# Performance work log

Measured on AMD Instinct MI355X. Metric: run time of the kernel, lower is better.

## Reference

```python
import jax, jax.numpy as jnp
import numpy as np


def setup_inputs() -> dict:
    key = jax.random.key(0)
    N, nH, D, L, P = 2, 8, 32, 4, 4
    shapes = np.array([[92, 92], [46, 46], [23, 23], [12, 12]], dtype=np.int64)
    areas = shapes[:, 0] * shapes[:, 1]
    Lin = int(areas.sum())  # 11253
    Lq = Lin  # encoder self-attention
    k1, k2, k3 = jax.random.split(key, 3)
    value = jax.random.normal(k1, (N, Lin, nH, D), dtype=jnp.float32)
    sampling_locations = jax.random.uniform(k2, (N, Lq, nH, L, P, 2), dtype=jnp.float32)
    aw = jax.random.uniform(k3, (N, Lq, nH, L, P), dtype=jnp.float32)
    attention_weights = aw / aw.sum(axis=(-2, -1), keepdims=True)  # softmax-normalized over L*P
    spatial_shapes = jnp.asarray(shapes)
    starts = np.concatenate([[0], np.cumsum(areas)[:-1]])
    level_start_index = jnp.asarray(starts, dtype=jnp.int64)
    return dict(value=value, spatial_shapes=spatial_shapes,
                level_start_index=level_start_index,
                sampling_locations=sampling_locations,
                attention_weights=attention_weights)


def _gather2d(v_nh, xi, yi, Hl, Wl):
    # v_nh: [N, nH, Hl*Wl, D]; xi, yi: [N, Lq, nH, P] int32 pixel coords
    N, Lq, nH, P = xi.shape
    valid = (xi >= 0) & (xi < Wl) & (yi >= 0) & (yi < Hl)
    xc = jnp.clip(xi, 0, Wl - 1)
    yc = jnp.clip(yi, 0, Hl - 1)
    idx = (yc * Wl + xc).transpose(0, 2, 1, 3).reshape(N, nH, Lq * P)
    vals = jax.vmap(jax.vmap(lambda v, i: v[i]))(v_nh, idx)  # [N, nH, Lq*P, D]
    vals = vals.reshape(N, nH, Lq, P, -1).transpose(0, 2, 1, 3, 4)  # [N, Lq, nH, P, D]
    return vals * valid[..., None].astype(vals.dtype)


def reference(value, spatial_shapes, level_start_index, sampling_locations, attention_weights):
    # ms_deform_attn core: per-level bilinear sampling (align_corners=False,
    # zero padding) at learned locations, weighted sum over levels and points.
    shapes_np = np.asarray(spatial_shapes)
    starts_np = np.asarray(level_start_index)
    N, Lin, nH, D = value.shape
    _, Lq, _, L, P, _ = sampling_locations.shape
    out = jnp.zeros((N, Lq, nH, D), dtype=value.dtype)
    for lvl in range(L):
        Hl, Wl = int(shapes_np[lvl, 0]), int(shapes_np[lvl, 1])
        s = int(starts_np[lvl])
        v_nh = value[:, s:s + Hl * Wl].transpose(0, 2, 1, 3)  # [N, nH, Hl*Wl, D]
        loc = sampling_locations[:, :, :, lvl]  # [N, Lq, nH, P, 2]
        # grid_sample convention: normalized [0,1] -> pixel coord, align_corners=False
        x = loc[..., 0] * Wl - 0.5
        y = loc[..., 1] * Hl - 0.5
        x0f = jnp.floor(x); y0f = jnp.floor(y)
        dx = x - x0f; dy = y - y0f
        x0 = x0f.astype(jnp.int32); y0 = y0f.astype(jnp.int32)
        x1 = x0 + 1; y1 = y0 + 1
        w00 = ((1.0 - dx) * (1.0 - dy))[..., None]
        w01 = (dx * (1.0 - dy))[..., None]
        w10 = ((1.0 - dx) * dy)[..., None]
        w11 = (dx * dy)[..., None]
        samp = (w00 * _gather2d(v_nh, x0, y0, Hl, Wl)
                + w01 * _gather2d(v_nh, x1, y0, Hl, Wl)
                + w10 * _gather2d(v_nh, x0, y1, Hl, Wl)
                + w11 * _gather2d(v_nh, x1, y1, Hl, Wl))  # [N, Lq, nH, P, D]
        aw_l = attention_weights[:, :, :, lvl]  # [N, Lq, nH, P]
        out = out + (samp * aw_l[..., None]).sum(axis=3)
    return out.reshape(N, Lq, nH * D)
```

## Files before the change

### kernel.cpp

```cpp
#include <hip/hip_runtime.h>

#define NH 8
#define DD 32
#define LL 4
#define PP 4

typedef float  f32x4  __attribute__((ext_vector_type(4)));
typedef float  f32x2  __attribute__((ext_vector_type(2)));
typedef int    i32x4  __attribute__((ext_vector_type(4)));
typedef _Float16 half4v __attribute__((ext_vector_type(4)));

__global__ __launch_bounds__(256) void conv_kernel(
    const float* __restrict__ value, _Float16* __restrict__ vh,
    int Lin, int spx, int nSlabs)
{
    const int xcd  = blockIdx.x & 7;
    const int blk  = blockIdx.x >> 3;
    const int sw   = blk % spx;
    const int seg  = blk / spx;
    const int slab = xcd * spx + sw;
    if (slab >= nSlabs) return;
    const int i = seg * 256 + threadIdx.x;
    if (i >= Lin * 8) return;
    const int d4  = i & 7;
    const int pos = i >> 3;
    const int n   = slab >> 3;
    const int h   = slab & 7;

    const f32x4 v = __builtin_nontemporal_load(
        (const f32x4*)(value + (((size_t)n * Lin + pos) * NH + h) * DD + d4 * 4));
    half4v o;
    o.x = (_Float16)v.x; o.y = (_Float16)v.y; o.z = (_Float16)v.z; o.w = (_Float16)v.w;
    *(half4v*)(vh + ((size_t)slab * Lin + pos) * DD + d4 * 4) = o;
}

#define FMAMIX_LO(ACC, DW, W) \
    asm("v_fma_mix_f32 %0, %1, %2, %0 op_sel:[0,0,0] op_sel_hi:[1,0,0]" \
        : "+v"(ACC) : "v"(DW), "v"(W))
#define FMAMIX_HI(ACC, DW, W) \
    asm("v_fma_mix_f32 %0, %1, %2, %0 op_sel:[1,0,0] op_sel_hi:[1,0,0]" \
        : "+v"(ACC) : "v"(DW), "v"(W))

#define SB() __builtin_amdgcn_sched_barrier(0)

__global__ __attribute__((amdgpu_flat_work_group_size(256, 256)))
__attribute__((amdgpu_waves_per_eu(4)))
void msda_fwd_h(
    const _Float16* __restrict__ vh,
    const int*   __restrict__ ssh,
    const int*   __restrict__ lsi,
    const float* __restrict__ sloc,
    const float* __restrict__ aw,
    float*       __restrict__ out,
    int N, int Lq, int Lin, int spx, int nSlabs)
{
    __shared__ i32x4 ent[32 * 39];

    const int xcd   = blockIdx.x & 7;
    const int blk   = blockIdx.x >> 3;
    const int sw    = blk % spx;
    const int chunk = blk / spx;
    const int slab  = xcd * spx + sw;
    if (slab >= nSlabs) return;

    const int t  = threadIdx.x;
    const int u  = t >> 3;
    const int j  = t & 7;
    const int q  = chunk * 32 + u;
    const int qc = min(q, Lq - 1);
    const int n  = slab >> 3;
    const int h  = slab & 7;

    {
        const size_t nqh = ((size_t)n * Lq + qc) * NH + h;
        const int l = j >> 1;
        const bool is64 = (ssh[1] == 0);
        const int W = is64 ? ssh[4 * l + 2] : ssh[2 * l + 1];
        const int H = is64 ? ssh[4 * l]     : ssh[2 * l];
        const int S = is64 ? lsi[2 * l]     : lsi[l];
        const f32x4 lc = __builtin_nontemporal_load((const f32x4*)sloc + nqh * 8 + j);
        const f32x2 av = __builtin_nontemporal_load((const f32x2*)aw + nqh * 8 + j);
        const float fW = (float)W, fH = (float)H;
        const int rowb  = W * (DD * 2);
        const int sbase = S * (DD * 2);
#pragma unroll
        for (int pt = 0; pt < 2; ++pt) {
            const float x  = lc[2 * pt]     * fW - 0.5f;
            const float y  = lc[2 * pt + 1] * fH - 0.5f;
            const float wq = av[pt];
            const float x0f = floorf(x), y0f = floorf(y);
            const int x0 = (int)x0f, y0 = (int)y0f;
            const float dx = x - x0f, dy = y - y0f;
            const int x1 = x0 + 1, y1 = y0 + 1;
            const bool vx0 = (x0 >= 0) & (x0 < W), vx1 = (x1 >= 0) & (x1 < W);
            const bool vy0 = (y0 >= 0) & (y0 < H), vy1 = (y1 >= 0) & (y1 < H);
            const int cx0 = min(max(x0, 0), W - 1), cx1 = min(max(x1, 0), W - 1);
            const int cy0 = min(max(y0, 0), H - 1), cy1 = min(max(y1, 0), H - 1);
            const float wx0 = (1.f - dx) * wq * (vx0 ? 1.f : 0.f);
            const float wx1 = dx         * wq * (vx1 ? 1.f : 0.f);
            const float ty  = (1.f - dy) * (vy0 ? 1.f : 0.f);
            const float by  = dy         * (vy1 ? 1.f : 0.f);
            const int rt = cy0 * rowb + sbase;
            const int rb = cy1 * rowb + sbase;
            i32x4 e0, e1;
            e0.x = rt + cx0 * (DD * 2);  e0.y = rb + cx0 * (DD * 2);
            e0.z = __float_as_int(wx0 * ty);  e0.w = __float_as_int(wx0 * by);
            e1.x = rt + cx1 * (DD * 2);  e1.y = rb + cx1 * (DD * 2);
            e1.z = __float_as_int(wx1 * ty);  e1.w = __float_as_int(wx1 * by);
            const int base = u * 39 + 5 * j + 2 * pt;
            ent[base]     = e0;
            ent[base + 1] = e1;
        }
    }
    __syncthreads();
    if (q >= Lq) return;

    const int side = j >> 2;
    const int cg   = j & 3;
    const char* __restrict__ sb =
        (const char*)vh + (size_t)slab * Lin * (DD * 2) + cg * 16;
    const int ub = u * 39 + side;

    float acc[8];
#pragma unroll
    for (int k = 0; k < 8; ++k) acc[k] = 0.f;

#define RD(b, E) { \
    E[0] = ent[ub + 10 * (b) + 0]; \
    E[1] = ent[ub + 10 * (b) + 2]; \
    E[2] = ent[ub + 10 * (b) + 5]; \
    E[3] = ent[ub + 10 * (b) + 7]; }
#define LD(E, V) _Pragma("unroll") \
    for (int i = 0; i < 4; ++i) { \
        V[2*i]   = *(const i32x4*)(sb + (unsigned)E[i].x); \
        V[2*i+1] = *(const i32x4*)(sb + (unsigned)E[i].y); }
#define AC(E, V) _Pragma("unroll") \
    for (int i = 0; i < 4; ++i) { \
        const float wt = __int_as_float(E[i].z); \
        const float wb = __int_as_float(E[i].w); \
        _Pragma("unroll") for (int d = 0; d < 4; ++d) { \
            FMAMIX_LO(acc[2*d],   V[2*i][d],   wt); \
            FMAMIX_HI(acc[2*d+1], V[2*i][d],   wt); \
            FMAMIX_LO(acc[2*d],   V[2*i+1][d], wb); \
            FMAMIX_HI(acc[2*d+1], V[2*i+1][d], wb); } }

    i32x4 E0[4], E1[4], E2[4], E3[4];
    i32x4 V0[8], V1[8];
    RD(0, E0) RD(1, E1)
    SB();
    LD(E0, V0) LD(E1, V1)
    SB();
    AC(E0, V0)
    RD(2, E2)
    SB();
    LD(E2, V0)
    SB();
    AC(E1, V1)
    RD(3, E3)
    SB();
    LD(E3, V1)
    SB();
    AC(E2, V0)
    AC(E3, V1)

#pragma unroll
    for (int k = 0; k < 8; ++k)
        acc[k] += __shfl_xor(acc[k], 4);

    f32x4 st;
    st.x = acc[side * 4 + 0];
    st.y = acc[side * 4 + 1];
    st.z = acc[side * 4 + 2];
    st.w = acc[side * 4 + 3];
    const size_t onqh = ((size_t)n * Lq + q) * NH + h;
    __builtin_nontemporal_store(st, (f32x4*)(out + onqh * DD + cg * 8 + side * 4));
}

__global__ __launch_bounds__(256) void msda_fwd_f32(
    const float* __restrict__ value,
    const int*   __restrict__ spatial_shapes,
    const int*   __restrict__ level_start,
    const float* __restrict__ sloc,
    const float* __restrict__ aw,
    float*       __restrict__ out,
    int N, int Lq, int Lin, int total)
{
    int tid = blockIdx.x * blockDim.x + threadIdx.x;
    if (tid >= total) return;
    const int c  = tid & 7;
    const int h  = (tid >> 3) & 7;
    const int nq = tid >> 6;
    const int n  = nq / Lq;
    const bool is64 = (spatial_shapes[1] == 0);
    int Hs[LL], Ws[LL], Ss[LL];
#pragma unroll
    for (int l = 0; l < LL; ++l) {
        if (is64) { Hs[l] = spatial_shapes[4*l]; Ws[l] = spatial_shapes[4*l+2]; Ss[l] = level_start[2*l]; }
        else      { Hs[l] = spatial_shapes[2*l]; Ws[l] = spatial_shapes[2*l+1]; Ss[l] = level_start[l]; }
    }
    const size_t nqh = (size_t)nq * NH + h;
    const float* loc_p = sloc + nqh * (LL * PP * 2);
    const float* aw_p  = aw   + nqh * (LL * PP);
    float4 acc = make_float4(0.f, 0.f, 0.f, 0.f);
#pragma unroll
    for (int l = 0; l < LL; ++l) {
        const int H = Hs[l], W = Ws[l];
        const float* vb = value + (((size_t)n * Lin + Ss[l]) * NH + h) * DD + c * 4;
#pragma unroll
        for (int p = 0; p < PP; ++p) {
            const int jj = l * PP + p;
            const float x = loc_p[2*jj] * (float)W - 0.5f;
            const float y = loc_p[2*jj+1] * (float)H - 0.5f;
            const float w = aw_p[jj];
            const float x0f = floorf(x), y0f = floorf(y);
            const int x0 = (int)x0f, y0 = (int)y0f, x1 = x0+1, y1 = y0+1;
            const float dx = x - x0f, dy = y - y0f;
            const bool vx0 = x0>=0 && x0<W, vx1 = x1>=0 && x1<W;
            const bool vy0 = y0>=0 && y0<H, vy1 = y1>=0 && y1<H;
            const int cx0 = min(max(x0,0),W-1), cx1 = min(max(x1,0),W-1);
            const int cy0 = min(max(y0,0),H-1), cy1 = min(max(y1,0),H-1);
            const float w00 = (1.f-dx)*(1.f-dy)*w*((vx0&&vy0)?1.f:0.f);
            const float w01 = dx*(1.f-dy)*w*((vx1&&vy0)?1.f:0.f);
            const float w10 = (1.f-dx)*dy*w*((vx0&&vy1)?1.f:0.f);
            const float w11 = dx*dy*w*((vx1&&vy1)?1.f:0.f);
            const float4 v00 = *(const float4*)(vb + (size_t)(cy0*W+cx0)*(NH*DD));
            const float4 v01 = *(const float4*)(vb + (size_t)(cy0*W+cx1)*(NH*DD));
            const float4 v10 = *(const float4*)(vb + (size_t)(cy1*W+cx0)*(NH*DD));
            const float4 v11 = *(const float4*)(vb + (size_t)(cy1*W+cx1)*(NH*DD));
            acc.x += w00*v00.x + w01*v01.x + w10*v10.x + w11*v11.x;
            acc.y += w00*v00.y + w01*v01.y + w10*v10.y + w11*v11.y;
            acc.z += w00*v00.z + w01*v01.z + w10*v10.z + w11*v11.z;
            acc.w += w00*v00.w + w01*v01.w + w10*v10.w + w11*v11.w;
        }
    }
    *(float4*)(out + nqh * DD + c * 4) = acc;
}

extern "C" void kernel_launch(void* const* d_in, const int* in_sizes, int n_in,
                              void* d_out, int out_size, void* d_ws, size_t ws_size,
                              hipStream_t stream)
{
    const float* value = (const float*)d_in[0];
    const int*   ss    = (const int*)  d_in[1];
    const int*   lsi   = (const int*)  d_in[2];
    const float* sloc  = (const float*)d_in[3];
    const float* aw    = (const float*)d_in[4];
    float* out = (float*)d_out;

    const int N = 2;
    const int Lq  = in_sizes[4] / (N * NH * LL * PP);
    const int Lin = in_sizes[0] / (N * NH * DD);

    const size_t need = (size_t)N * NH * Lin * DD * sizeof(_Float16);
    if (ws_size >= need) {
        _Float16* vh = (_Float16*)d_ws;
        const int nSlabs = N * NH;
        const int spx    = (nSlabs + 7) / 8;
        const int segs   = (Lin * 8 + 255) / 256;
        conv_kernel<<<8 * spx * segs, 256, 0, stream>>>(value, vh, Lin, spx, nSlabs);

        const int chunks = (Lq + 31) / 32;
        const int grid   = 8 * spx * chunks;
        msda_fwd_h<<<grid, 256, 0, stream>>>(vh, ss, lsi, sloc, aw, out,
                                             N, Lq, Lin, spx, nSlabs);
    } else {
        const int total = N * Lq * NH * 8;
        msda_fwd_f32<<<(total + 255) / 256, 256, 0, stream>>>(value, ss, lsi, sloc, aw, out,
                                                              N, Lq, Lin, total);
    }
}
```

Before: 131.7 us.

## Stage small pyramid levels of value slab into LDS for gathers

Copies the fp16 value data for levels 2 and 3 (the small 23x23 and 12x12 maps, about 42 KB per head slab) into shared memory at block start. Gathers for those levels then read LDS instead of global memory, while levels 0 and 1 still gather from global memory. The gather schedule is restructured so the global loads for levels 0/1 are in flight while the LDS-based accumulation runs. Waves-per-EU drops to 2 to fit the large LDS footprint. The cost is an extra bulk copy per block of 32 queries and lower occupancy.

Result: slower. 148.2 us (+12.6%).

```diff
diff --git a/kernel.cpp b/kernel.cpp
--- a/kernel.cpp
+++ b/kernel.cpp
@@ -4,6 +4,7 @@
 #define DD 32
 #define LL 4
 #define PP 4
+#define STAGE_BYTES 43072
 
 typedef float  f32x4  __attribute__((ext_vector_type(4)));
 typedef float  f32x2  __attribute__((ext_vector_type(2)));
@@ -44,7 +45,7 @@
 #define SB() __builtin_amdgcn_sched_barrier(0)
 
 __global__ __attribute__((amdgpu_flat_work_group_size(256, 256)))
-__attribute__((amdgpu_waves_per_eu(4)))
+__attribute__((amdgpu_waves_per_eu(2)))
 void msda_fwd_h(
     const _Float16* __restrict__ vh,
     const int*   __restrict__ ssh,
@@ -55,6 +56,7 @@
     int N, int Lq, int Lin, int spx, int nSlabs)
 {
     __shared__ i32x4 ent[32 * 39];
+    __shared__ i32x4 stage4[STAGE_BYTES / 16];
 
     const int xcd   = blockIdx.x & 7;
     const int blk   = blockIdx.x >> 3;
@@ -71,10 +73,29 @@
     const int n  = slab >> 3;
     const int h  = slab & 7;
 
+    const bool is64 = (ssh[1] == 0);
+    const int  S2v  = is64 ? lsi[4] : lsi[2];
+    const int  stB  = (Lin - S2v) * (DD * 2);
+    const bool staged = (stB > 0) && (stB <= STAGE_BYTES);
+
+    if (staged) {
+        const char* src = (const char*)vh + ((size_t)slab * Lin + S2v) * (DD * 2);
+        i32x4 tmp[11];
+#pragma unroll
+        for (int k = 0; k < 11; ++k) {
+            const int off = t * 16 + k * 4096;
+            if (off < stB) tmp[k] = *(const i32x4*)(src + off);
+        }
+#pragma unroll
+        for (int k = 0; k < 11; ++k) {
+            const int off = t * 16 + k * 4096;
+            if (off < stB) *(i32x4*)((char*)stage4 + off) = tmp[k];
+        }
+    }
+
     {
         const size_t nqh = ((size_t)n * Lq + qc) * NH + h;
         const int l = j >> 1;
-        const bool is64 = (ssh[1] == 0);
         const int W = is64 ? ssh[4 * l + 2] : ssh[2 * l + 1];
         const int H = is64 ? ssh[4 * l]     : ssh[2 * l];
         const int S = is64 ? lsi[2 * l]     : lsi[l];
@@ -82,7 +103,7 @@
         const f32x2 av = __builtin_nontemporal_load((const f32x2*)aw + nqh * 8 + j);
         const float fW = (float)W, fH = (float)H;
         const int rowb  = W * (DD * 2);
-        const int sbase = S * (DD * 2);
+        const int sbase = (staged && j >= 4) ? (S - S2v) * (DD * 2) : S * (DD * 2);
 #pragma unroll
         for (int pt = 0; pt < 2; ++pt) {
             const float x  = lc[2 * pt]     * fW - 0.5f;
@@ -119,6 +140,7 @@
     const int cg   = j & 3;
     const char* __restrict__ sb =
         (const char*)vh + (size_t)slab * Lin * (DD * 2) + cg * 16;
+    const char* __restrict__ stg = (const char*)stage4 + cg * 16;
     const int ub = u * 39 + side;
 
     float acc[8];
@@ -134,6 +156,10 @@
     for (int i = 0; i < 4; ++i) { \
         V[2*i]   = *(const i32x4*)(sb + (unsigned)E[i].x); \
         V[2*i+1] = *(const i32x4*)(sb + (unsigned)E[i].y); }
+#define LLD(E, V) _Pragma("unroll") \
+    for (int i = 0; i < 4; ++i) { \
+        V[2*i]   = *(const i32x4*)(stg + (unsigned)E[i].x); \
+        V[2*i+1] = *(const i32x4*)(stg + (unsigned)E[i].y); }
 #define AC(E, V) _Pragma("unroll") \
     for (int i = 0; i < 4; ++i) { \
         const float wt = __int_as_float(E[i].z); \
@@ -150,18 +176,31 @@
     SB();
     LD(E0, V0) LD(E1, V1)
     SB();
-    AC(E0, V0)
-    RD(2, E2)
-    SB();
-    LD(E2, V0)
-    SB();
-    AC(E1, V1)
-    RD(3, E3)
-    SB();
-    LD(E3, V1)
-    SB();
-    AC(E2, V0)
-    AC(E3, V1)
+    if (staged) {
+        i32x4 VL[8];
+        RD(2, E2)
+        LLD(E2, VL)
+        AC(E2, VL)
+        RD(3, E3)
+        LLD(E3, VL)
+        AC(E3, VL)
+        SB();
+        AC(E0, V0)
+        AC(E1, V1)
+    } else {
+        AC(E0, V0)
+        RD(2, E2)
+        SB();
+        LD(E2, V0)
+        SB();
+        AC(E1, V1)
+        RD(3, E3)
+        SB();
+        LD(E3, V1)
+        SB();
+        AC(E2, V0)
+        AC(E3, V1)
+    }
 
 #pragma unroll
     for (int k = 0; k < 8; ++k)
```
